# Kernel tuning notes

Measured on AMD Instinct MI355X. Metric: run time of the kernel, lower is better.

The kernel has to match this reference:

```python
import jax, jax.numpy as jnp
import numpy as np

N = 8192          # number of latent vectors z
M = 16384         # number of KDE sample points (multiple of N_EMB)
N_EMB = 16        # n_embeddings on the circle
Z_DIM = 2         # fixed by get_embeddings (cos/sin stack)
INIT_LOG_SIGMA = 0.0


def setup_inputs() -> dict:
    key = jax.random.key(0)
    k1, k2 = jax.random.split(key)
    z = jax.random.normal(k1, (N, Z_DIM), dtype=jnp.float32)
    eps = jax.random.normal(k2, (M // N_EMB, Z_DIM), dtype=jnp.float32)
    # get_embeddings: points on a circle of radius 4
    angles = jnp.linspace(0.0, 2.0 * np.pi, N_EMB)
    embeddings = (jnp.stack([jnp.cos(angles), jnp.sin(angles)], axis=1) * 4.0).astype(jnp.float32)
    log_sigma = jnp.full((1,), INIT_LOG_SIGMA, dtype=jnp.float32)
    temperature = jnp.full((1,), 0.5, dtype=jnp.float32)
    return {"z": z, "embeddings": embeddings, "log_sigma": log_sigma,
            "eps": eps, "temperature": temperature}


def reference(z, embeddings, log_sigma, eps, temperature):
    T = temperature[0]
    ls = log_sigma[0]
    sigma = jnp.exp(ls)
    z_dim = z.shape[1]
    n = z.shape[0]
    # mean: (n_emb, D); samples e: (n_emb * M//n_emb, D) == (M, D)
    mean = (1.0 - T) * embeddings
    e = (mean[:, None, :] + eps[None, :, :] * T).reshape(-1, z_dim)
    # squared euclidean distance (N, M) via gemm expansion (same math as ||z-e||^2)
    d = (jnp.sum(z * z, axis=1)[:, None]
         + jnp.sum(e * e, axis=1)[None, :]
         - 2.0 * (z @ e.T))
    alpha = -1.0 / (2.0 * sigma ** 2)
    lse = jax.nn.logsumexp(alpha * d, axis=0)  # reduce over N -> (M,)
    # np.log(np.e) == 1.0
    loss = (-jnp.mean(lse)
            + 0.5 * z_dim * (2.0 * ls - 1.0)
            + jnp.log(jnp.float32(n)))
    return loss
```

## Files before the change

kernel.cpp:

```cpp
#include <hip/hip_runtime.h>
#include <math.h>

#define N_TOT 8192
#define M_TOT 16384
#define EPS_N 1024
#define N_EMB 16

#define LOG2E 1.4426950408889634f
#define LN2   0.6931471805599453f
#define EXP2(x) __builtin_amdgcn_exp2f(x)
#define LOG2F_(x) __builtin_amdgcn_logf(x)

#define BLOCK 256
#define IC    64
#define NICH  (N_TOT / IC)
#define LCH   256
#define NLCH  (EPS_N / LCH)

__global__ __launch_bounds__(BLOCK) void gemm_partial_kernel(
    const float* __restrict__ z, const float* __restrict__ emb,
    const float* __restrict__ log_sigma, const float* __restrict__ eps,
    const float* __restrict__ temperature, float* __restrict__ part,
    unsigned int* __restrict__ cnt)
{
    __shared__ float4 rows[IC * 5];
    __shared__ float red[4][N_EMB * 128];

    const int t  = threadIdx.x;
    const int l0 = blockIdx.x * LCH;
    const int ib = blockIdx.y;

    if (t == 0 && blockIdx.x == 0 && blockIdx.y == 0)
        cnt[0] = 0u;

    const float ls = log_sigma[0];
    const float T  = temperature[0];
    const float alpha = -0.5f * EXP2(LOG2E * (-2.0f * ls));
    const float La  = LOG2E * alpha;
    const float omT = 1.0f - T;

    {
        const int il = t & (IC - 1);
        const int kq = t >> 6;
        const int i  = ib * IC + il;
        const float z0 = z[2 * i], z1 = z[2 * i + 1];
        const float c  = La * (z0 * z0 + z1 * z1);
        const float b0 = -2.0f * La * z0, b1 = -2.0f * La * z1;
        float4 pa;
#pragma unroll
        for (int kk = 0; kk < 4; ++kk) {
            int k = kq * 4 + kk;
            float m0 = omT * emb[2 * k], m1 = omT * emb[2 * k + 1];
            ((float*)&pa)[kk] = EXP2(c + b0 * m0 + b1 * m1);
        }
        rows[il * 5 + kq] = pa;
        if (kq == 0)
            rows[il * 5 + 4] = make_float4(T * b0, T * b1, 0.0f, 0.0f);
    }

    const int lane = t & 63;
    const int w    = t >> 6;
    const float2* eps2 = (const float2*)eps;
    const float2 ua = eps2[l0 + lane];
    const float2 ub = eps2[l0 + 64 + lane];
    const float2 uc = eps2[l0 + 128 + lane];
    const float2 ud = eps2[l0 + 192 + lane];

    __syncthreads();

    float sa[N_EMB] = {0.0f};
    float sb[N_EMB] = {0.0f};
    float sc_[N_EMB] = {0.0f};
    float sd[N_EMB] = {0.0f};
#pragma unroll 2
    for (int n = 0; n < IC / 4; ++n) {
        const int ir = w * (IC / 4) + n;
        float4 p0 = rows[ir * 5 + 0];
        float4 p1 = rows[ir * 5 + 1];
        float4 p2 = rows[ir * 5 + 2];
        float4 p3 = rows[ir * 5 + 3];
        float4 tb = rows[ir * 5 + 4];
        float qa = EXP2(fmaf(tb.y, ua.y, tb.x * ua.x));
        float qb = EXP2(fmaf(tb.y, ub.y, tb.x * ub.x));
        float qc = EXP2(fmaf(tb.y, uc.y, tb.x * uc.x));
        float qd = EXP2(fmaf(tb.y, ud.y, tb.x * ud.x));
        float pk[16];
        *(float4*)&pk[0]  = p0; *(float4*)&pk[4]  = p1;
        *(float4*)&pk[8]  = p2; *(float4*)&pk[12] = p3;
#pragma unroll
        for (int k = 0; k < N_EMB; ++k) {
            sa[k]  = fmaf(pk[k], qa, sa[k]);
            sb[k]  = fmaf(pk[k], qb, sb[k]);
            sc_[k] = fmaf(pk[k], qc, sc_[k]);
            sd[k]  = fmaf(pk[k], qd, sd[k]);
        }
    }

#pragma unroll
    for (int k = 0; k < N_EMB; ++k) {
        red[w][k * 128 + lane]      = sa[k];
        red[w][k * 128 + 64 + lane] = sb[k];
    }
    __syncthreads();
#pragma unroll
    for (int r = 0; r < (N_EMB * 128) / BLOCK; ++r) {
        const int e  = t + r * BLOCK;
        const float S = red[0][e] + red[1][e] + red[2][e] + red[3][e];
        const int k  = e >> 7;
        const int ll = e & 127;
        part[ib * M_TOT + k * EPS_N + l0 + ll] = S;
    }
    __syncthreads();
#pragma unroll
    for (int k = 0; k < N_EMB; ++k) {
        red[w][k * 128 + lane]      = sc_[k];
        red[w][k * 128 + 64 + lane] = sd[k];
    }
    __syncthreads();
#pragma unroll
    for (int r = 0; r < (N_EMB * 128) / BLOCK; ++r) {
        const int e  = t + r * BLOCK;
        const float S = red[0][e] + red[1][e] + red[2][e] + red[3][e];
        const int k  = e >> 7;
        const int ll = e & 127;
        part[ib * M_TOT + k * EPS_N + l0 + 128 + ll] = S;
    }
}

__global__ __launch_bounds__(BLOCK) void reduce_final_kernel(
    const float* __restrict__ emb, const float* __restrict__ log_sigma,
    const float* __restrict__ eps, const float* __restrict__ temperature,
    const float* __restrict__ part, float* __restrict__ bsum,
    unsigned int* __restrict__ cnt, float* __restrict__ out)
{
    const int j = blockIdx.x * BLOCK + threadIdx.x;
    const float ls = log_sigma[0];
    const float T  = temperature[0];
    const float alpha = -0.5f * EXP2(LOG2E * (-2.0f * ls));

    float S = 0.0f;
#pragma unroll 16
    for (int ib = 0; ib < NICH; ++ib)
        S += part[ib * M_TOT + j];

    const int k = j >> 10, l = j & (EPS_N - 1);
    const float omT = 1.0f - T;
    const float e0 = omT * emb[2 * k]     + T * eps[2 * l];
    const float e1 = omT * emb[2 * k + 1] + T * eps[2 * l + 1];
    const float g  = LOG2E * alpha * (e0 * e0 + e1 * e1);

    float v = g + LOG2F_(S);

#pragma unroll
    for (int off = 32; off; off >>= 1) v += __shfl_down(v, off, 64);
    __shared__ float wsum[BLOCK / 64];
    __shared__ unsigned int sdone;
    const int lane = threadIdx.x & 63, w = threadIdx.x >> 6;
    if (lane == 0) wsum[w] = v;
    __syncthreads();

    if (threadIdx.x == 0) {
        const float b = wsum[0] + wsum[1] + wsum[2] + wsum[3];
        __hip_atomic_store(&bsum[blockIdx.x], b, __ATOMIC_RELAXED,
                           __HIP_MEMORY_SCOPE_AGENT);
        asm volatile("s_waitcnt vmcnt(0)" ::: "memory");
        const unsigned int old = __hip_atomic_fetch_add(
            &cnt[0], 1u, __ATOMIC_RELAXED, __HIP_MEMORY_SCOPE_AGENT);
        sdone = (old == (unsigned int)(M_TOT / BLOCK - 1)) ? 1u : 0u;
    }
    __syncthreads();
    if (sdone == 0u) return;

    if (threadIdx.x < 64) {
        float v2 = __hip_atomic_load(&bsum[threadIdx.x], __ATOMIC_RELAXED,
                                     __HIP_MEMORY_SCOPE_AGENT);
#pragma unroll
        for (int off = 32; off; off >>= 1) v2 += __shfl_down(v2, off, 64);
        if (threadIdx.x == 0) {
            const float sum_lse = v2 * LN2;
            out[0] = -sum_lse / (float)M_TOT + (2.0f * ls - 1.0f)
                     + 9.010913347279288f;
        }
    }
}

extern "C" void kernel_launch(void* const* d_in, const int* in_sizes, int n_in,
                              void* d_out, int out_size, void* d_ws, size_t ws_size,
                              hipStream_t stream)
{
    const float* z    = (const float*)d_in[0];
    const float* emb  = (const float*)d_in[1];
    const float* lsig = (const float*)d_in[2];
    const float* eps  = (const float*)d_in[3];
    const float* temp = (const float*)d_in[4];

    unsigned int* cnt = (unsigned int*)d_ws;
    float* bsum = (float*)d_ws + 16;
    float* part = (float*)d_ws + 128;

    dim3 grid1(NLCH, NICH);
    gemm_partial_kernel<<<grid1, BLOCK, 0, stream>>>(z, emb, lsig, eps, temp,
                                                     part, cnt);
    reduce_final_kernel<<<M_TOT / BLOCK, BLOCK, 0, stream>>>(
        emb, lsig, eps, temp, part, bsum, cnt, (float*)d_out);
}
```

Before: 75.64 us.

## Double row chunk per block, vectorize partial reduction, split-N final reduce

The GEMM kernel now handles 128 z rows per block using 512 threads, which halves the number of partial rows written to and read back from the workspace. The cross-wave reduction is vectorized to float4 LDS reads and global stores. The final kernel splits the summation over row chunks across four waves per 64 columns and combines them in LDS, giving more blocks and more memory-level parallelism for that reduction. The trade-offs are a larger LDS footprint, fewer GEMM blocks (256), and a 256-entry bsum that now needs the workspace offset moved.

Result: faster. 73.46 us (-2.9%).

```diff
diff --git a/kernel.cpp b/kernel.cpp
--- a/kernel.cpp
+++ b/kernel.cpp
@@ -11,8 +11,8 @@
 #define EXP2(x) __builtin_amdgcn_exp2f(x)
 #define LOG2F_(x) __builtin_amdgcn_logf(x)
 
-#define BLOCK 256
-#define IC    64
+#define BLOCK 512
+#define IC    128
 #define NICH  (N_TOT / IC)
 #define LCH   256
 #define NLCH  (EPS_N / LCH)
@@ -23,8 +23,9 @@
     const float* __restrict__ temperature, float* __restrict__ part,
     unsigned int* __restrict__ cnt)
 {
-    __shared__ float4 rows[IC * 5];
-    __shared__ float red[4][N_EMB * 128];
+    __shared__ float4 rowsP[IC][4];
+    __shared__ float2 tbv[IC];
+    __shared__ float  red[8][N_EMB * 128];
 
     const int t  = threadIdx.x;
     const int l0 = blockIdx.x * LCH;
@@ -41,11 +42,11 @@
 
     {
         const int il = t & (IC - 1);
-        const int kq = t >> 6;
+        const int kq = t >> 7;
         const int i  = ib * IC + il;
-        const float z0 = z[2 * i], z1 = z[2 * i + 1];
-        const float c  = La * (z0 * z0 + z1 * z1);
-        const float b0 = -2.0f * La * z0, b1 = -2.0f * La * z1;
+        const float2 zi = ((const float2*)z)[i];
+        const float c  = La * (zi.x * zi.x + zi.y * zi.y);
+        const float b0 = -2.0f * La * zi.x, b1 = -2.0f * La * zi.y;
         float4 pa;
 #pragma unroll
         for (int kk = 0; kk < 4; ++kk) {
@@ -53,9 +54,9 @@
             float m0 = omT * emb[2 * k], m1 = omT * emb[2 * k + 1];
             ((float*)&pa)[kk] = EXP2(c + b0 * m0 + b1 * m1);
         }
-        rows[il * 5 + kq] = pa;
+        rowsP[il][kq] = pa;
         if (kq == 0)
-            rows[il * 5 + 4] = make_float4(T * b0, T * b1, 0.0f, 0.0f);
+            tbv[il] = make_float2(T * b0, T * b1);
     }
 
     const int lane = t & 63;
@@ -73,13 +74,13 @@
     float sc_[N_EMB] = {0.0f};
     float sd[N_EMB] = {0.0f};
 #pragma unroll 2
-    for (int n = 0; n < IC / 4; ++n) {
-        const int ir = w * (IC / 4) + n;
-        float4 p0 = rows[ir * 5 + 0];
-        float4 p1 = rows[ir * 5 + 1];
-        float4 p2 = rows[ir * 5 + 2];
-        float4 p3 = rows[ir * 5 + 3];
-        float4 tb = rows[ir * 5 + 4];
+    for (int n = 0; n < IC / 8; ++n) {
+        const int ir = w * (IC / 8) + n;
+        float4 p0 = rowsP[ir][0];
+        float4 p1 = rowsP[ir][1];
+        float4 p2 = rowsP[ir][2];
+        float4 p3 = rowsP[ir][3];
+        float2 tb = tbv[ir];
         float qa = EXP2(fmaf(tb.y, ua.y, tb.x * ua.x));
         float qb = EXP2(fmaf(tb.y, ub.y, tb.x * ub.x));
         float qc = EXP2(fmaf(tb.y, uc.y, tb.x * uc.x));
@@ -102,13 +103,16 @@
         red[w][k * 128 + 64 + lane] = sb[k];
     }
     __syncthreads();
-#pragma unroll
-    for (int r = 0; r < (N_EMB * 128) / BLOCK; ++r) {
-        const int e  = t + r * BLOCK;
-        const float S = red[0][e] + red[1][e] + red[2][e] + red[3][e];
-        const int k  = e >> 7;
-        const int ll = e & 127;
-        part[ib * M_TOT + k * EPS_N + l0 + ll] = S;
+    {
+        const int e = t * 4;
+        float4 S = *(const float4*)&red[0][e];
+#pragma unroll
+        for (int ww = 1; ww < 8; ++ww) {
+            const float4 a = *(const float4*)&red[ww][e];
+            S.x += a.x; S.y += a.y; S.z += a.z; S.w += a.w;
+        }
+        const int base = ib * M_TOT + (e >> 7) * EPS_N + l0 + (e & 127);
+        *(float4*)&part[base] = S;
     }
     __syncthreads();
 #pragma unroll
@@ -117,67 +121,75 @@
         red[w][k * 128 + 64 + lane] = sd[k];
     }
     __syncthreads();
-#pragma unroll
-    for (int r = 0; r < (N_EMB * 128) / BLOCK; ++r) {
-        const int e  = t + r * BLOCK;
-        const float S = red[0][e] + red[1][e] + red[2][e] + red[3][e];
-        const int k  = e >> 7;
-        const int ll = e & 127;
-        part[ib * M_TOT + k * EPS_N + l0 + 128 + ll] = S;
+    {
+        const int e = t * 4;
+        float4 S = *(const float4*)&red[0][e];
+#pragma unroll
+        for (int ww = 1; ww < 8; ++ww) {
+            const float4 a = *(const float4*)&red[ww][e];
+            S.x += a.x; S.y += a.y; S.z += a.z; S.w += a.w;
+        }
+        const int base = ib * M_TOT + (e >> 7) * EPS_N + l0 + 128 + (e & 127);
+        *(float4*)&part[base] = S;
     }
 }
 
-__global__ __launch_bounds__(BLOCK) void reduce_final_kernel(
+#define K2BLOCK 256
+__global__ __launch_bounds__(K2BLOCK) void reduce_final_kernel(
     const float* __restrict__ emb, const float* __restrict__ log_sigma,
     const float* __restrict__ eps, const float* __restrict__ temperature,
     const float* __restrict__ part, float* __restrict__ bsum,
     unsigned int* __restrict__ cnt, float* __restrict__ out)
 {
-    const int j = blockIdx.x * BLOCK + threadIdx.x;
+    const int lane = threadIdx.x & 63;
+    const int w    = threadIdx.x >> 6;
+    const int j    = blockIdx.x * 64 + lane;
+
     const float ls = log_sigma[0];
     const float T  = temperature[0];
     const float alpha = -0.5f * EXP2(LOG2E * (-2.0f * ls));
 
-    float S = 0.0f;
-#pragma unroll 16
-    for (int ib = 0; ib < NICH; ++ib)
-        S += part[ib * M_TOT + j];
-
+    float Sp = 0.0f;
+#pragma unroll
+    for (int n = 0; n < NICH / 4; ++n)
+        Sp += part[(w * (NICH / 4) + n) * M_TOT + j];
+
+    __shared__ float red2[4][64];
+    __shared__ unsigned int sdone;
+    red2[w][lane] = Sp;
+    __syncthreads();
+
+    const float S = ((red2[0][lane] + red2[1][lane]) + red2[2][lane]) + red2[3][lane];
     const int k = j >> 10, l = j & (EPS_N - 1);
     const float omT = 1.0f - T;
     const float e0 = omT * emb[2 * k]     + T * eps[2 * l];
     const float e1 = omT * emb[2 * k + 1] + T * eps[2 * l + 1];
     const float g  = LOG2E * alpha * (e0 * e0 + e1 * e1);
-
     float v = g + LOG2F_(S);
-
 #pragma unroll
     for (int off = 32; off; off >>= 1) v += __shfl_down(v, off, 64);
-    __shared__ float wsum[BLOCK / 64];
-    __shared__ unsigned int sdone;
-    const int lane = threadIdx.x & 63, w = threadIdx.x >> 6;
-    if (lane == 0) wsum[w] = v;
-    __syncthreads();
 
     if (threadIdx.x == 0) {
-        const float b = wsum[0] + wsum[1] + wsum[2] + wsum[3];
-        __hip_atomic_store(&bsum[blockIdx.x], b, __ATOMIC_RELAXED,
+        __hip_atomic_store(&bsum[blockIdx.x], v, __ATOMIC_RELAXED,
                            __HIP_MEMORY_SCOPE_AGENT);
         asm volatile("s_waitcnt vmcnt(0)" ::: "memory");
         const unsigned int old = __hip_atomic_fetch_add(
             &cnt[0], 1u, __ATOMIC_RELAXED, __HIP_MEMORY_SCOPE_AGENT);
-        sdone = (old == (unsigned int)(M_TOT / BLOCK - 1)) ? 1u : 0u;
+        sdone = (old == (unsigned int)(M_TOT / 64 - 1)) ? 1u : 0u;
     }
     __syncthreads();
     if (sdone == 0u) return;
 
     if (threadIdx.x < 64) {
-        float v2 = __hip_atomic_load(&bsum[threadIdx.x], __ATOMIC_RELAXED,
-                                     __HIP_MEMORY_SCOPE_AGENT);
-#pragma unroll
-        for (int off = 32; off; off >>= 1) v2 += __shfl_down(v2, off, 64);
-        if (threadIdx.x == 0) {
-            const float sum_lse = v2 * LN2;
+        float q0 = __hip_atomic_load(&bsum[lane],       __ATOMIC_RELAXED, __HIP_MEMORY_SCOPE_AGENT);
+        float q1 = __hip_atomic_load(&bsum[lane + 64],  __ATOMIC_RELAXED, __HIP_MEMORY_SCOPE_AGENT);
+        float q2 = __hip_atomic_load(&bsum[lane + 128], __ATOMIC_RELAXED, __HIP_MEMORY_SCOPE_AGENT);
+        float q3 = __hip_atomic_load(&bsum[lane + 192], __ATOMIC_RELAXED, __HIP_MEMORY_SCOPE_AGENT);
+        float q  = ((q0 + q1) + q2) + q3;
+#pragma unroll
+        for (int off = 32; off; off >>= 1) q += __shfl_down(q, off, 64);
+        if (lane == 0) {
+            const float sum_lse = q * LN2;
             out[0] = -sum_lse / (float)M_TOT + (2.0f * ls - 1.0f)
                      + 9.010913347279288f;
         }
@@ -196,11 +208,11 @@
 
     unsigned int* cnt = (unsigned int*)d_ws;
     float* bsum = (float*)d_ws + 16;
-    float* part = (float*)d_ws + 128;
+    float* part = (float*)d_ws + 512;
 
     dim3 grid1(NLCH, NICH);
     gemm_partial_kernel<<<grid1, BLOCK, 0, stream>>>(z, emb, lsig, eps, temp,
                                                      part, cnt);
-    reduce_final_kernel<<<M_TOT / BLOCK, BLOCK, 0, stream>>>(
+    reduce_final_kernel<<<M_TOT / 64, K2BLOCK, 0, stream>>>(
         emb, lsig, eps, temp, part, bsum, cnt, (float*)d_out);
 }
```
